# Kernel optimization log

Measured on AMD Instinct MI355X. Metric: run time of the kernel, lower is better.

The kernel has to match this reference:

```python
import jax, jax.numpy as jnp
import numpy as np

RES = (256, 256, 256)
CH = 16
RR = 8  # ceil(log2(256))
N_PTS = 262144


def grid_sample_2d(plane, gx, gy):
    """Bilinear grid_sample, align_corners=True.
    plane: (C, H, W); gx in [-1,1] indexes W, gy indexes H. Returns (N, C)."""
    C, H, W = plane.shape
    ix = (gx + 1.0) * 0.5 * (W - 1)
    iy = (gy + 1.0) * 0.5 * (H - 1)
    x0f = jnp.floor(ix)
    y0f = jnp.floor(iy)
    wx = ix - x0f
    wy = iy - y0f
    x0 = jnp.clip(x0f.astype(jnp.int32), 0, W - 1)
    x1 = jnp.clip(x0 + 1, 0, W - 1)
    y0 = jnp.clip(y0f.astype(jnp.int32), 0, H - 1)
    y1 = jnp.clip(y0 + 1, 0, H - 1)
    v00 = plane[:, y0, x0]  # (C, N)
    v01 = plane[:, y0, x1]
    v10 = plane[:, y1, x0]
    v11 = plane[:, y1, x1]
    out = (v00 * (1 - wx) * (1 - wy) + v01 * wx * (1 - wy)
           + v10 * (1 - wx) * wy + v11 * wx * wy)
    return out.T  # (N, C)


def integrate(P, coords):
    """P: (N, 2*CH, RR) with real part channels [:CH], imag [CH:].
    coords: (N,) in [-1,1]. Fourier-basis numerical integration (real part)."""
    c = (coords + 1.0) * 0.5 * (2 ** RR - 1)  # (N,)
    coef = jnp.concatenate([jnp.zeros((1,), jnp.float32),
                            2.0 ** jnp.arange(RR - 1, dtype=jnp.float32)]) / (2 ** RR)
    theta = 2.0 * jnp.pi * c[:, None] * coef  # (N, RR)
    # Re(exp(i*theta) . P_complex) = cos.Re(P) - sin.Im(P)
    re = jnp.einsum('nr,ncr->nc', jnp.cos(theta), P[:, :CH, :])
    im = jnp.einsum('nr,ncr->nc', jnp.sin(theta), P[:, CH:, :])
    return re - im  # (N, CH)


def setup_inputs() -> dict:
    key = jax.random.key(0)
    k0, k1, k2, k3 = jax.random.split(key, 4)
    inputs = jax.random.uniform(k0, (N_PTS, 3), dtype=jnp.float32,
                                minval=-1.0, maxval=1.0)
    C = 2 * RR * CH
    Pu = 0.001 * jax.random.normal(k1, (1, C, RES[1], RES[2]), dtype=jnp.float32)
    Pv = 0.001 * jax.random.normal(k2, (1, C, RES[0], RES[2]), dtype=jnp.float32)
    Pw = 0.001 * jax.random.normal(k3, (1, C, RES[0], RES[1]), dtype=jnp.float32)
    return {"inputs": inputs, "Pu": Pu, "Pv": Pv, "Pw": Pw}


def reference(inputs, Pu, Pv, Pw):
    c0, c1, c2 = inputs[:, 0], inputs[:, 1], inputs[:, 2]
    # grid last-dim (x,y): x indexes width (last plane axis), y the height.
    su = grid_sample_2d(Pu[0], c1, c2).reshape(-1, 2 * CH, RR)
    sv = grid_sample_2d(Pv[0], c0, c2).reshape(-1, 2 * CH, RR)
    sw = grid_sample_2d(Pw[0], c0, c1).reshape(-1, 2 * CH, RR)
    return integrate(su, c0) + integrate(sv, c1) + integrate(sw, c2)  # (N, CH)
```

## Files before the change

kernel.cpp:

```cpp
#include <hip/hip_runtime.h>
#include <hip/hip_fp16.h>
#include <math.h>

#define NPTS 262144
#define PLANE_ELEMS 16777216u

typedef __attribute__((ext_vector_type(4))) float f4;
typedef __attribute__((ext_vector_type(4))) unsigned int u4;

#define OFF_SORTED   (3ull * PLANE_ELEMS * 2ull)
#define OFF_PARTIAL  (OFF_SORTED + (size_t)3 * NPTS * 16)
#define OFF_HIST     (OFF_PARTIAL + (size_t)3 * NPTS * 16 * 2)
#define WS_NEED      (OFF_HIST + (size_t)3 * 65536 * 4)

__device__ __forceinline__ void plane_xy(int p, float c0, float c1, float c2,
                                         float& gx, float& gy, float& ax) {
  if (p == 0)      { gx = c1; gy = c2; ax = c0; }
  else if (p == 1) { gx = c0; gy = c2; ax = c1; }
  else             { gx = c0; gy = c1; ax = c2; }
}

__device__ __forceinline__ int cell_of(float g) {
  float i = (g + 1.f) * 0.5f * 255.f;
  int x0 = (int)floorf(i);
  return x0 < 0 ? 0 : (x0 > 255 ? 255 : x0);
}

__device__ __forceinline__ void trans_load(const float* __restrict__ src,
                                           unsigned c0, unsigned hw0, int tid,
                                           f4 (&va)[4], f4 (&vb)[4]) {
#pragma unroll
  for (int j = 0; j < 4; ++j) {
    int idx = j * 256 + tid;
    int rp = idx >> 5;
    int q = idx & 31;
    const f4* base = (const f4*)(src + (size_t)(c0 + 2 * rp) * 65536u + hw0 + 4 * q);
    va[j] = __builtin_nontemporal_load(base);
    vb[j] = __builtin_nontemporal_load(base + 16384);
  }
}

__device__ __forceinline__ void trans_proc(unsigned* tile, __half* dst,
                                           unsigned c0, unsigned hw0, int tid,
                                           f4 (&va)[4], f4 (&vb)[4]) {
#pragma unroll
  for (int j = 0; j < 4; ++j) {
    int idx = j * 256 + tid;
    int rp = idx >> 5;
    int q = idx & 31;
#pragma unroll
    for (int k = 0; k < 4; ++k) {
      int hw = 4 * q + k;
      __half2 h = __floats2half2_rn(va[j][k], vb[j][k]);
      tile[hw * 36 + (rp ^ (hw >> 3))] = *(unsigned*)&h;
    }
  }
  __syncthreads();
  int seg = tid & 7;
#pragma unroll
  for (int jj = 0; jj < 4; ++jj) {
    int hw = jj * 32 + (tid >> 3);
    int s = hw >> 3;
    u4 v = *(const u4*)(tile + hw * 36 + 4 * ((seg ^ (s >> 2)) & 7));
    u4 o;
    switch (s & 3) {
      case 0: o = v; break;
      case 1: o = u4{v.y, v.x, v.w, v.z}; break;
      case 2: o = u4{v.z, v.w, v.x, v.y}; break;
      default: o = u4{v.w, v.z, v.y, v.x}; break;
    }
    *(u4*)((char*)dst + ((size_t)(hw0 + hw) * 256u + c0) * 2u + seg * 16u) = o;
  }
  __syncthreads();
}

__global__ __launch_bounds__(256) void PREFFFT_trans_k(
    const float* __restrict__ Pu, const float* __restrict__ Pv,
    const float* __restrict__ Pw, __half* __restrict__ dst0) {
  __shared__ unsigned tile[128 * 36];
  const float* src = blockIdx.z == 0 ? Pu : (blockIdx.z == 1 ? Pv : Pw);
  __half* dst = dst0 + (size_t)blockIdx.z * PLANE_ELEMS;
  const unsigned hwbase = blockIdx.x * 512u;
  const unsigned c0 = blockIdx.y * 64u;
  const int tid = threadIdx.x;

  f4 vaA[4], vbA[4], vaB[4], vbB[4];
  trans_load(src, c0, hwbase, tid, vaA, vbA);
  trans_load(src, c0, hwbase + 128u, tid, vaB, vbB);
  trans_proc(tile, dst, c0, hwbase, tid, vaA, vbA);
  trans_load(src, c0, hwbase + 256u, tid, vaA, vbA);
  trans_proc(tile, dst, c0, hwbase + 128u, tid, vaB, vbB);
  trans_load(src, c0, hwbase + 384u, tid, vaB, vbB);
  trans_proc(tile, dst, c0, hwbase + 256u, tid, vaA, vbA);
  trans_proc(tile, dst, c0, hwbase + 384u, tid, vaB, vbB);
}

__global__ __launch_bounds__(256) void PREFFFT_hist_k(
    const float* __restrict__ inputs, unsigned* __restrict__ hist) {
  int n = blockIdx.x * 256 + threadIdx.x;
  int p = blockIdx.y;
  float c0 = inputs[n * 3 + 0], c1 = inputs[n * 3 + 1], c2 = inputs[n * 3 + 2];
  float gx, gy, ax;
  plane_xy(p, c0, c1, c2, gx, gy, ax);
  int key = (cell_of(gy) << 8) | cell_of(gx);
  atomicAdd(&hist[p * 65536 + key], 1u);
}

__global__ __launch_bounds__(1024) void PREFFFT_scan_k(unsigned* __restrict__ hist) {
  __shared__ unsigned part[1024];
  unsigned* h = hist + (size_t)blockIdx.x * 65536;
  int t = threadIdx.x;
  unsigned s = 0;
#pragma unroll 8
  for (int i = 0; i < 64; ++i) s += h[t * 64 + i];
  part[t] = s;
  __syncthreads();
  for (int off = 1; off < 1024; off <<= 1) {
    unsigned v = (t >= off) ? part[t - off] : 0u;
    __syncthreads();
    part[t] += v;
    __syncthreads();
  }
  unsigned run = (t == 0) ? 0u : part[t - 1];
#pragma unroll 8
  for (int i = 0; i < 64; ++i) {
    unsigned c = h[t * 64 + i];
    h[t * 64 + i] = run;
    run += c;
  }
}

__global__ __launch_bounds__(256) void PREFFFT_scat_k(
    const float* __restrict__ inputs, unsigned* __restrict__ hist,
    float4* __restrict__ sortedC) {
  int n = blockIdx.x * 256 + threadIdx.x;
  int p = blockIdx.y;
  float c0 = inputs[n * 3 + 0], c1 = inputs[n * 3 + 1], c2 = inputs[n * 3 + 2];
  float gx, gy, ax;
  plane_xy(p, c0, c1, c2, gx, gy, ax);
  int key = (cell_of(gy) << 8) | cell_of(gx);
  unsigned pos = atomicAdd(&hist[p * 65536 + key], 1u);
  sortedC[(size_t)p * NPTS + pos] =
      make_float4(gx, gy, ax, __uint_as_float((unsigned)n));
}

__global__ __launch_bounds__(256) void PREFFFT_samp_k(
    const float4* __restrict__ sortedC, const __half* __restrict__ T,
    __half* __restrict__ partial) {
  int p = blockIdx.y;
  int bx = blockIdx.x;
  int lbx = (bx & 7) * 1024 + (bx >> 3);
  int slot = lbx * 32 + ((int)threadIdx.x >> 3);
  int t = threadIdx.x & 7;

  float4 sc = sortedC[(size_t)p * NPTS + slot];
  unsigned n = __float_as_uint(sc.w);
  float gx = sc.x, gy = sc.y, ax = sc.z;

  float ix = (gx + 1.f) * 0.5f * 255.f;
  float iy = (gy + 1.f) * 0.5f * 255.f;
  float x0f = floorf(ix), y0f = floorf(iy);
  float wx = ix - x0f, wy = iy - y0f;
  int x0 = (int)x0f; x0 = x0 < 0 ? 0 : (x0 > 255 ? 255 : x0);
  int y0 = (int)y0f; y0 = y0 < 0 ? 0 : (y0 > 255 ? 255 : y0);
  int x1 = x0 + 1 > 255 ? 255 : x0 + 1;
  int y1 = y0 + 1 > 255 ? 255 : y0 + 1;
  float w00 = (1.f - wx) * (1.f - wy);
  float w01 = wx * (1.f - wy);
  float w10 = (1.f - wx) * wy;
  float w11 = wx * wy;

  const __half* __restrict__ P = T + (size_t)p * PLANE_ELEMS;
  int r00 = (y0 * 256 + x0) * 256, r01 = (y0 * 256 + x1) * 256;
  int r10 = (y1 * 256 + x0) * 256, r11 = (y1 * 256 + x1) * 256;
  int ore = t * 16;
  int oim = 128 + t * 16;

  f4 a0 = *(const f4*)(P + r00 + ore),     a1 = *(const f4*)(P + r00 + ore + 8);
  f4 a2 = *(const f4*)(P + r00 + oim),     a3 = *(const f4*)(P + r00 + oim + 8);
  f4 b0 = *(const f4*)(P + r01 + ore),     b1 = *(const f4*)(P + r01 + ore + 8);
  f4 b2 = *(const f4*)(P + r01 + oim),     b3 = *(const f4*)(P + r01 + oim + 8);
  f4 c0v = *(const f4*)(P + r10 + ore),    c1v = *(const f4*)(P + r10 + ore + 8);
  f4 c2v = *(const f4*)(P + r10 + oim),    c3v = *(const f4*)(P + r10 + oim + 8);
  f4 d0 = *(const f4*)(P + r11 + ore),     d1 = *(const f4*)(P + r11 + ore + 8);
  f4 d2 = *(const f4*)(P + r11 + oim),     d3 = *(const f4*)(P + r11 + oim + 8);

  __half2 hw00 = __float2half2_rn(w00), hw01 = __float2half2_rn(w01);
  __half2 hw10 = __float2half2_rn(w10), hw11 = __float2half2_rn(w11);

  __half2 bre[8], bim[8];
#pragma unroll
  for (int q = 0; q < 4; ++q) {
    __half2 v;
    v = __hmul2(((const __half2*)&a0)[q], hw00);
    v = __hfma2(((const __half2*)&b0)[q],  hw01, v);
    v = __hfma2(((const __half2*)&c0v)[q], hw10, v);
    bre[q] = __hfma2(((const __half2*)&d0)[q], hw11, v);

    v = __hmul2(((const __half2*)&a1)[q], hw00);
    v = __hfma2(((const __half2*)&b1)[q],  hw01, v);
    v = __hfma2(((const __half2*)&c1v)[q], hw10, v);
    bre[q + 4] = __hfma2(((const __half2*)&d1)[q], hw11, v);

    v = __hmul2(((const __half2*)&a2)[q], hw00);
    v = __hfma2(((const __half2*)&b2)[q],  hw01, v);
    v = __hfma2(((const __half2*)&c2v)[q], hw10, v);
    bim[q] = __hfma2(((const __half2*)&d2)[q], hw11, v);

    v = __hmul2(((const __half2*)&a3)[q], hw00);
    v = __hfma2(((const __half2*)&b3)[q],  hw01, v);
    v = __hfma2(((const __half2*)&c3v)[q], hw10, v);
    bim[q + 4] = __hfma2(((const __half2*)&d3)[q], hw11, v);
  }

  float fre[16], fim[16];
#pragma unroll
  for (int q = 0; q < 8; ++q) {
    float2 vr = __half22float2(bre[q]);
    float2 vi = __half22float2(bim[q]);
    fre[2 * q] = vr.x; fre[2 * q + 1] = vr.y;
    fim[2 * q] = vi.x; fim[2 * q + 1] = vi.y;
  }

  float cs = (ax + 1.f) * 0.5f * 255.f;
  float th = 6.283185307179586f * cs * (1.f / 256.f);
  float s, c;
  __sincosf(th, &s, &c);
  float aR0 = fre[0], aR1 = fre[8];
  float aI0 = 0.f,    aI1 = 0.f;
#pragma unroll
  for (int r = 1; r < 8; ++r) {
    aR0 += fre[r] * c;     aR1 += fre[8 + r] * c;
    aI0 += fim[r] * s;     aI1 += fim[8 + r] * s;
    if (r < 7) {
      float c2 = c + c;
      float cn = c2 * c - 1.f;
      s = c2 * s;
      c = cn;
    }
  }

  *(__half2*)(partial + ((size_t)p * NPTS + n) * 16 + 2 * t) =
      __floats2half2_rn(aR0 - aI0, aR1 - aI1);
}

__global__ __launch_bounds__(256) void PREFFFT_red_k(
    const __half* __restrict__ part, float* __restrict__ out) {
  size_t i = (size_t)blockIdx.x * 256 + threadIdx.x;
  const size_t PS = (size_t)NPTS * 16;
  union H8 { u4 v; __half2 h[4]; };
  H8 a, b, c;
  a.v = *(const u4*)(part + i * 8);
  b.v = *(const u4*)(part + PS + i * 8);
  c.v = *(const u4*)(part + 2 * PS + i * 8);
  f4 o0, o1;
#pragma unroll
  for (int k = 0; k < 4; ++k) {
    float2 fa = __half22float2(a.h[k]);
    float2 fb = __half22float2(b.h[k]);
    float2 fc = __half22float2(c.h[k]);
    float lo = fa.x + fb.x + fc.x;
    float hi = fa.y + fb.y + fc.y;
    if (k < 2) { o0[2 * k] = lo; o0[2 * k + 1] = hi; }
    else       { o1[2 * (k - 2)] = lo; o1[2 * (k - 2) + 1] = hi; }
  }
  ((f4*)out)[i * 2] = o0;
  ((f4*)out)[i * 2 + 1] = o1;
}

__global__ __launch_bounds__(256) void PREFFFT_fallback_k(
    const float* __restrict__ inputs, const float* __restrict__ Tu,
    const float* __restrict__ Tv, const float* __restrict__ Tw,
    float* __restrict__ out) {
  int gtid = blockIdx.x * 256 + threadIdx.x;
  int n = gtid >> 5;
  int t = threadIdx.x & 31;
  const bool is_re = t < 16;
  float c0 = inputs[n * 3 + 0], c1 = inputs[n * 3 + 1], c2 = inputs[n * 3 + 2];
  const float* PL[3] = {Tu, Tv, Tw};
  float acc = 0.f;
#pragma unroll
  for (int p = 0; p < 3; ++p) {
    float gx, gy, ax;
    plane_xy(p, c0, c1, c2, gx, gy, ax);
    float ix = (gx + 1.f) * 0.5f * 255.f;
    float iy = (gy + 1.f) * 0.5f * 255.f;
    float x0f = floorf(ix), y0f = floorf(iy);
    float wx = ix - x0f, wy = iy - y0f;
    int x0 = (int)x0f; x0 = x0 < 0 ? 0 : (x0 > 255 ? 255 : x0);
    int y0 = (int)y0f; y0 = y0 < 0 ? 0 : (y0 > 255 ? 255 : y0);
    int x1 = x0 + 1 > 255 ? 255 : x0 + 1;
    int y1 = y0 + 1 > 255 ? 255 : y0 + 1;
    float w00 = (1.f - wx) * (1.f - wy), w01 = wx * (1.f - wy);
    float w10 = (1.f - wx) * wy, w11 = wx * wy;
    int i00 = y0 * 256 + x0, i01 = y0 * 256 + x1;
    int i10 = y1 * 256 + x0, i11 = y1 * 256 + x1;
    float b[8];
#pragma unroll
    for (int j = 0; j < 8; ++j) {
      const float* base = PL[p] + (size_t)(t * 8 + j) * 65536u;
      b[j] = w00 * base[i00] + w01 * base[i01] + w10 * base[i10] + w11 * base[i11];
    }
    float csv = (ax + 1.f) * 0.5f * 255.f;
    float theta1 = 6.283185307179586f * csv * (1.f / 256.f);
    float partial = is_re ? b[0] : 0.f;
#pragma unroll
    for (int r = 1; r < 8; ++r) {
      float thr = theta1 * (float)(1 << (r - 1));
      float s, c;
      __sincosf(thr, &s, &c);
      partial += b[r] * (is_re ? c : s);
    }
    float other = __shfl_xor(partial, 16);
    acc += partial - other;
  }
  if (is_re) out[n * 16 + t] = acc;
}

extern "C" void kernel_launch(void* const* d_in, const int* in_sizes, int n_in,
                              void* d_out, int out_size, void* d_ws, size_t ws_size,
                              hipStream_t stream) {
  const float* inputs = (const float*)d_in[0];
  const float* Pu = (const float*)d_in[1];
  const float* Pv = (const float*)d_in[2];
  const float* Pw = (const float*)d_in[3];
  float* out = (float*)d_out;

  if (ws_size >= WS_NEED) {
    char* ws = (char*)d_ws;
    __half*   T       = (__half*)ws;
    float4*   sortedC = (float4*)(ws + OFF_SORTED);
    __half*   partial = (__half*)(ws + OFF_PARTIAL);
    unsigned* hist    = (unsigned*)(ws + OFF_HIST);

    {
      dim3 tg(128, 4, 3);
      PREFFFT_trans_k<<<tg, 256, 0, stream>>>(Pu, Pv, Pw, T);
    }
    hipMemsetAsync(hist, 0, (size_t)3 * 65536 * 4, stream);
    {
      dim3 tg(NPTS / 256, 3);
      PREFFFT_hist_k<<<tg, 256, 0, stream>>>(inputs, hist);
    }
    PREFFFT_scan_k<<<3, 1024, 0, stream>>>(hist);
    {
      dim3 tg(NPTS / 256, 3);
      PREFFFT_scat_k<<<tg, 256, 0, stream>>>(inputs, hist, sortedC);
    }
    {
      dim3 tg(NPTS / 32, 3);
      PREFFFT_samp_k<<<tg, 256, 0, stream>>>(sortedC, T, partial);
    }
    PREFFFT_red_k<<<2048, 256, 0, stream>>>(partial, out);
  } else {
    PREFFFT_fallback_k<<<NPTS / 8, 256, 0, stream>>>(inputs, Pu, Pv, Pw, out);
  }
}
```

Before: 231.5 us.

## Fuse plane transpose with histogram kernel and scatter point indices only

Merges the plane-transpose kernel and the histogram kernel into one launch, with block ranges split between the two tasks, so the cheap histogram work overlaps the bandwidth-heavy transpose and one launch disappears. The scatter pass now writes a 4-byte point index instead of a 16-byte float4 of coordinates, and the sampling kernel gathers the coordinates from the original inputs through that index. This cuts scatter write traffic but adds a dependent indirect load in the sampling kernel.

```diff
diff --git a/kernel.cpp b/kernel.cpp
--- a/kernel.cpp
+++ b/kernel.cpp
@@ -8,8 +8,8 @@
 typedef __attribute__((ext_vector_type(4))) float f4;
 typedef __attribute__((ext_vector_type(4))) unsigned int u4;
 
-#define OFF_SORTED   (3ull * PLANE_ELEMS * 2ull)
-#define OFF_PARTIAL  (OFF_SORTED + (size_t)3 * NPTS * 16)
+#define OFF_IDX      (3ull * PLANE_ELEMS * 2ull)
+#define OFF_PARTIAL  (OFF_IDX + (size_t)3 * NPTS * 4)
 #define OFF_HIST     (OFF_PARTIAL + (size_t)3 * NPTS * 16 * 2)
 #define WS_NEED      (OFF_HIST + (size_t)3 * 65536 * 4)
 
@@ -74,36 +74,45 @@
   __syncthreads();
 }
 
-__global__ __launch_bounds__(256) void PREFFFT_trans_k(
+__global__ __launch_bounds__(256) void PREFFFT_fat1_k(
     const float* __restrict__ Pu, const float* __restrict__ Pv,
-    const float* __restrict__ Pw, __half* __restrict__ dst0) {
+    const float* __restrict__ Pw, __half* __restrict__ dst0,
+    const float* __restrict__ inputs, unsigned* __restrict__ hist) {
   __shared__ unsigned tile[128 * 36];
-  const float* src = blockIdx.z == 0 ? Pu : (blockIdx.z == 1 ? Pv : Pw);
-  __half* dst = dst0 + (size_t)blockIdx.z * PLANE_ELEMS;
-  const unsigned hwbase = blockIdx.x * 512u;
-  const unsigned c0 = blockIdx.y * 64u;
+  const int bx = blockIdx.x;
   const int tid = threadIdx.x;
-
-  f4 vaA[4], vbA[4], vaB[4], vbB[4];
-  trans_load(src, c0, hwbase, tid, vaA, vbA);
-  trans_load(src, c0, hwbase + 128u, tid, vaB, vbB);
-  trans_proc(tile, dst, c0, hwbase, tid, vaA, vbA);
-  trans_load(src, c0, hwbase + 256u, tid, vaA, vbA);
-  trans_proc(tile, dst, c0, hwbase + 128u, tid, vaB, vbB);
-  trans_load(src, c0, hwbase + 384u, tid, vaB, vbB);
-  trans_proc(tile, dst, c0, hwbase + 256u, tid, vaA, vbA);
-  trans_proc(tile, dst, c0, hwbase + 384u, tid, vaB, vbB);
-}
-
-__global__ __launch_bounds__(256) void PREFFFT_hist_k(
-    const float* __restrict__ inputs, unsigned* __restrict__ hist) {
-  int n = blockIdx.x * 256 + threadIdx.x;
-  int p = blockIdx.y;
-  float c0 = inputs[n * 3 + 0], c1 = inputs[n * 3 + 1], c2 = inputs[n * 3 + 2];
-  float gx, gy, ax;
-  plane_xy(p, c0, c1, c2, gx, gy, ax);
-  int key = (cell_of(gy) << 8) | cell_of(gx);
-  atomicAdd(&hist[p * 65536 + key], 1u);
+  if (bx < 1536) {
+    int bz = bx / 512;
+    int rem = bx - bz * 512;
+    int by = rem >> 7;
+    int bxx = rem & 127;
+    const float* src = bz == 0 ? Pu : (bz == 1 ? Pv : Pw);
+    __half* dst = dst0 + (size_t)bz * PLANE_ELEMS;
+    const unsigned hwbase = bxx * 512u;
+    const unsigned c0 = by * 64u;
+    f4 vaA[4], vbA[4], vaB[4], vbB[4];
+    trans_load(src, c0, hwbase, tid, vaA, vbA);
+    trans_load(src, c0, hwbase + 128u, tid, vaB, vbB);
+    trans_proc(tile, dst, c0, hwbase, tid, vaA, vbA);
+    trans_load(src, c0, hwbase + 256u, tid, vaA, vbA);
+    trans_proc(tile, dst, c0, hwbase + 128u, tid, vaB, vbB);
+    trans_load(src, c0, hwbase + 384u, tid, vaB, vbB);
+    trans_proc(tile, dst, c0, hwbase + 256u, tid, vaA, vbA);
+    trans_proc(tile, dst, c0, hwbase + 384u, tid, vaB, vbB);
+  } else {
+    int hb = bx - 1536;
+#pragma unroll
+    for (int it = 0; it < 4; ++it) {
+      int item = hb * 1024 + it * 256 + tid;
+      int n = item & (NPTS - 1);
+      int p = item >> 18;
+      float c0 = inputs[n * 3 + 0], c1 = inputs[n * 3 + 1], c2 = inputs[n * 3 + 2];
+      float gx, gy, ax;
+      plane_xy(p, c0, c1, c2, gx, gy, ax);
+      int key = (cell_of(gy) << 8) | cell_of(gx);
+      atomicAdd(&hist[p * 65536 + key], 1u);
+    }
+  }
 }
 
 __global__ __launch_bounds__(1024) void PREFFFT_scan_k(unsigned* __restrict__ hist) {
@@ -132,7 +141,7 @@
 
 __global__ __launch_bounds__(256) void PREFFFT_scat_k(
     const float* __restrict__ inputs, unsigned* __restrict__ hist,
-    float4* __restrict__ sortedC) {
+    unsigned* __restrict__ idx) {
   int n = blockIdx.x * 256 + threadIdx.x;
   int p = blockIdx.y;
   float c0 = inputs[n * 3 + 0], c1 = inputs[n * 3 + 1], c2 = inputs[n * 3 + 2];
@@ -140,22 +149,22 @@
   plane_xy(p, c0, c1, c2, gx, gy, ax);
   int key = (cell_of(gy) << 8) | cell_of(gx);
   unsigned pos = atomicAdd(&hist[p * 65536 + key], 1u);
-  sortedC[(size_t)p * NPTS + pos] =
-      make_float4(gx, gy, ax, __uint_as_float((unsigned)n));
+  idx[(size_t)p * NPTS + pos] = (unsigned)n;
 }
 
 __global__ __launch_bounds__(256) void PREFFFT_samp_k(
-    const float4* __restrict__ sortedC, const __half* __restrict__ T,
-    __half* __restrict__ partial) {
+    const unsigned* __restrict__ idx, const float* __restrict__ inputs,
+    const __half* __restrict__ T, __half* __restrict__ partial) {
   int p = blockIdx.y;
   int bx = blockIdx.x;
   int lbx = (bx & 7) * 1024 + (bx >> 3);
   int slot = lbx * 32 + ((int)threadIdx.x >> 3);
   int t = threadIdx.x & 7;
 
-  float4 sc = sortedC[(size_t)p * NPTS + slot];
-  unsigned n = __float_as_uint(sc.w);
-  float gx = sc.x, gy = sc.y, ax = sc.z;
+  unsigned n = idx[(size_t)p * NPTS + slot];
+  float c0 = inputs[n * 3 + 0], c1 = inputs[n * 3 + 1], c2 = inputs[n * 3 + 2];
+  float gx, gy, ax;
+  plane_xy(p, c0, c1, c2, gx, gy, ax);
 
   float ix = (gx + 1.f) * 0.5f * 255.f;
   float iy = (gy + 1.f) * 0.5f * 255.f;
@@ -329,27 +338,20 @@
   if (ws_size >= WS_NEED) {
     char* ws = (char*)d_ws;
     __half*   T       = (__half*)ws;
-    float4*   sortedC = (float4*)(ws + OFF_SORTED);
+    unsigned* idx     = (unsigned*)(ws + OFF_IDX);
     __half*   partial = (__half*)(ws + OFF_PARTIAL);
     unsigned* hist    = (unsigned*)(ws + OFF_HIST);
 
-    {
-      dim3 tg(128, 4, 3);
-      PREFFFT_trans_k<<<tg, 256, 0, stream>>>(Pu, Pv, Pw, T);
-    }
     hipMemsetAsync(hist, 0, (size_t)3 * 65536 * 4, stream);
-    {
-      dim3 tg(NPTS / 256, 3);
-      PREFFFT_hist_k<<<tg, 256, 0, stream>>>(inputs, hist);
-    }
+    PREFFFT_fat1_k<<<2304, 256, 0, stream>>>(Pu, Pv, Pw, T, inputs, hist);
     PREFFFT_scan_k<<<3, 1024, 0, stream>>>(hist);
     {
       dim3 tg(NPTS / 256, 3);
-      PREFFFT_scat_k<<<tg, 256, 0, stream>>>(inputs, hist, sortedC);
+      PREFFFT_scat_k<<<tg, 256, 0, stream>>>(inputs, hist, idx);
     }
     {
       dim3 tg(NPTS / 32, 3);
-      PREFFFT_samp_k<<<tg, 256, 0, stream>>>(sortedC, T, partial);
+      PREFFFT_samp_k<<<tg, 256, 0, stream>>>(idx, inputs, T, partial);
     }
     PREFFFT_red_k<<<2048, 256, 0, stream>>>(partial, out);
   } else {
```

Result: faster. 213.6 us (-7.7%).
